# Kernel optimization log

Hardware: AMD Instinct MI355X
Metric: run time of the kernel (lower is better)

The kernel has to match this reference:

```python
import jax, jax.numpy as jnp
import numpy as np

B, S, D, H = 4, 2048, 1024, 16
HD = D // H
NEG = -1e30


def setup_inputs() -> dict:
    key = jax.random.key(0)
    ks = jax.random.split(key, 6)
    scale = 1.0 / np.sqrt(D)
    return {
        "q": jax.random.normal(ks[0], (B, S, D), jnp.float32),
        "k": jax.random.normal(ks[1], (B, S, D), jnp.float32),
        "v": jax.random.normal(ks[2], (B, S, D), jnp.float32),
        "mask": jnp.ones((B, 1, S), jnp.float32),
        "wq": jax.random.normal(ks[3], (D, D), jnp.float32) * scale,
        "bq": jnp.zeros((D,), jnp.float32),
        "wk": jax.random.normal(ks[4], (D, D), jnp.float32) * scale,
        "bk": jnp.zeros((D,), jnp.float32),
        "wv": jax.random.normal(ks[5], (D, D), jnp.float32) * scale,
        "bv": jnp.zeros((D,), jnp.float32),
    }


def _heads(x):
    # (B,S,D) -> (B,H,S,HD)
    return x.reshape(B, S, H, HD).transpose(0, 2, 1, 3)


def reference(q, k, v, mask, wq, bq, wk, bk, wv, bv):
    # pointwise Conv1D(kernel=1) == linear: x @ W^T + b (W: (out,in))
    qh = _heads(jnp.einsum('bsd,ed->bse', q, wq) + bq)
    kh = _heads(jnp.einsum('bsd,ed->bse', k, wk) + bk)
    vh = _heads(jnp.einsum('bsd,ed->bse', v, wv) + bv)
    scores = jnp.einsum('bhqd,bhkd->bhqk', qh, kh) / jnp.sqrt(jnp.float32(HD))
    # mask_logits: x + (1 - mask) * -1e30, mask (B,1,S) -> (B,1,1,S)
    scores = scores + (1.0 - mask[:, None, :, :]) * NEG
    probs = jax.nn.softmax(scores, axis=-1)  # dropout is identity in eval
    ctx = jnp.einsum('bhqk,bhkd->bhqd', probs, vh)
    return ctx.transpose(0, 2, 1, 3).reshape(B, S, D)
```

## Files before the change

kernel.cpp:

```cpp
#include <hip/hip_runtime.h>
#include <math.h>

typedef __attribute__((ext_vector_type(8)))  _Float16 f16x8;
typedef __attribute__((ext_vector_type(4)))  _Float16 f16x4;
typedef __attribute__((ext_vector_type(2)))  __fp16   h16x2;
typedef __attribute__((ext_vector_type(4)))  float    f32x4;
typedef __attribute__((ext_vector_type(16))) float    f32x16;
typedef unsigned int u32;

static constexpr int B  = 4;
static constexpr int S  = 2048;
static constexpr int D  = 1024;
static constexpr int H  = 16;
static constexpr int HD = 64;

#define CSCALE 0.18033688011112042f
#define MSHIFT -5.770780163555854f

union U64cvt { f16x4 h; ushort4 u; };
union W4 { u32 w[4]; f16x8 v; };

__device__ __forceinline__ void gld16(const void* g, void* l) {
    __builtin_amdgcn_global_load_lds((const u32*)g, (u32*)l, 16, 0, 0);
}

__device__ __forceinline__ void cvtwr16(const float4& x, const float4& y, void* dst) {
    W4 w;
    w.w[0] = __builtin_bit_cast(u32, __builtin_amdgcn_cvt_pkrtz(x.x, x.y));
    w.w[1] = __builtin_bit_cast(u32, __builtin_amdgcn_cvt_pkrtz(x.z, x.w));
    w.w[2] = __builtin_bit_cast(u32, __builtin_amdgcn_cvt_pkrtz(y.x, y.y));
    w.w[3] = __builtin_bit_cast(u32, __builtin_amdgcn_cvt_pkrtz(y.z, y.w));
    *(f16x8*)dst = w.v;
}

__global__ __launch_bounds__(256)
void cvt_prep(const float* __restrict__ q, const float* __restrict__ k,
              const float* __restrict__ v,
              const float* __restrict__ wq, const float* __restrict__ wk,
              const float* __restrict__ wv,
              unsigned short* __restrict__ dst)
{
    const int c = blockIdx.x * 256 + threadIdx.x;
    const float* src;
    size_t idx;
    if (c < 3145728) {
        const int a = c >> 20;
        src = (a == 0) ? q : (a == 1) ? k : v;
        idx = (size_t)(c & 1048575) * 8;
    } else {
        const int c2 = c - 3145728;
        const int a = c2 >> 17;
        src = (a == 0) ? wq : (a == 1) ? wk : wv;
        idx = (size_t)(c2 & 131071) * 8;
    }
    const float4 x = *(const float4*)(src + idx);
    const float4 y = *(const float4*)(src + idx + 4);
    cvtwr16(x, y, dst + (size_t)c * 8);
}

__global__ __launch_bounds__(256)
void mf_prep(const float* __restrict__ mask, unsigned short* __restrict__ mf)
{
    const int cm   = blockIdx.x * 256 + threadIdx.x;
    const int b    = cm >> 12;
    const int rem  = cm & 4095;
    const int t    = rem >> 7;
    const int kb   = (rem >> 6) & 1;
    const int lane = rem & 63;
    const int kv   = t * 64 + kb * 32 + (lane & 31);
    const float m  = fmaf(1.0f - mask[(size_t)b * S + kv], -30000.0f, MSHIFT);
    W4 w;
    w.w[0] = __builtin_bit_cast(u32, __builtin_amdgcn_cvt_pkrtz(m, 0.0f));
    w.w[1] = 0; w.w[2] = 0; w.w[3] = 0;
    *(f16x8*)(mf + (size_t)cm * 8) = w.v;
}

__global__ __launch_bounds__(256)
void proj_f16(const unsigned short* __restrict__ af16,
              const unsigned short* __restrict__ wf16,
              const float* __restrict__ bqp, const float* __restrict__ bkp,
              const float* __restrict__ bvp,
              unsigned short* __restrict__ outs)
{
    const int bid = blockIdx.x;
    const int xcd = bid & 7;
    const int idx = bid >> 3;
    const int z   = idx / 64;
    const int r2  = idx - z * 64;
    const int mpl = r2 >> 3;
    const int np  = r2 & 7;
    const int mp  = (xcd >> 1) * 16 + (xcd & 1) * 8 + mpl;
    const int m0  = mp * 128;
    const int n0  = np * 128;

    const unsigned short* A  = af16 + (size_t)z * 8388608;
    const unsigned short* Wf = wf16 + (size_t)z * 1048576;
    const float* bias = (z == 0) ? bqp : (z == 1) ? bkp : bvp;
    unsigned short* out = outs + (size_t)z * 8388608;

    const int tid  = threadIdx.x;
    const int lane = tid & 63;
    const int wid  = tid >> 6;
    const int wr   = wid >> 1;
    const int wc   = wid & 1;

    __shared__ __align__(16) unsigned char lA[2][8192];
    __shared__ __align__(16) unsigned char lB[2][8192];

    f32x4 acc[4][4];
#pragma unroll
    for (int i = 0; i < 4; ++i)
#pragma unroll
        for (int j = 0; j < 4; ++j) acc[i][j] = (f32x4){0.f, 0.f, 0.f, 0.f};

    int grow[2], gcol[2], lbase[2];
#pragma unroll
    for (int i = 0; i < 2; ++i) {
        const int c = tid + 256 * i;
        grow[i]  = c >> 2;
        gcol[i]  = ((c & 3) - (grow[i] >> 1)) & 3;
        lbase[i] = (c & ~63) * 16;
    }

#pragma unroll
    for (int i = 0; i < 2; ++i) {
        gld16(A  + (size_t)(m0 + grow[i]) * D + gcol[i] * 8, lA[0] + lbase[i]);
        gld16(Wf + (size_t)(n0 + grow[i]) * D + gcol[i] * 8, lB[0] + lbase[i]);
    }
    __syncthreads();

    for (int kt = 0; kt < 32; ++kt) {
        const int cb = kt & 1, nx = cb ^ 1;

        if (kt < 31) {
            const int k1 = (kt + 1) * 32;
#pragma unroll
            for (int i = 0; i < 2; ++i) {
                gld16(A  + (size_t)(m0 + grow[i]) * D + k1 + gcol[i] * 8, lA[nx] + lbase[i]);
                gld16(Wf + (size_t)(n0 + grow[i]) * D + k1 + gcol[i] * 8, lB[nx] + lbase[i]);
            }
        }

        f16x8 af[4], bf[4];
#pragma unroll
        for (int mi = 0; mi < 4; ++mi) {
            const int row = wr * 64 + mi * 16 + (lane & 15);
            const int cc  = ((lane >> 4) + (row >> 1)) & 3;
            af[mi] = *(const f16x8*)(lA[cb] + row * 64 + cc * 16);
        }
#pragma unroll
        for (int ni = 0; ni < 4; ++ni) {
            const int row = wc * 64 + ni * 16 + (lane & 15);
            const int cc  = ((lane >> 4) + (row >> 1)) & 3;
            bf[ni] = *(const f16x8*)(lB[cb] + row * 64 + cc * 16);
        }

        __builtin_amdgcn_s_setprio(1);
#pragma unroll
        for (int mi = 0; mi < 4; ++mi)
#pragma unroll
            for (int ni = 0; ni < 4; ++ni)
                acc[mi][ni] = __builtin_amdgcn_mfma_f32_16x16x32_f16(af[mi], bf[ni], acc[mi][ni], 0, 0, 0);
        __builtin_amdgcn_s_setprio(0);

        __syncthreads();
    }

#pragma unroll
    for (int mi = 0; mi < 4; ++mi) {
        const int gmBase = m0 + wr * 64 + mi * 16 + ((lane >> 4) << 2);
        const int b  = gmBase >> 11;
        const int s0 = gmBase & 2047;
        const int tV   = s0 >> 6;
        const int kv6  = s0 & 63;
        const int ksg  = kv6 >> 4;
        const int hi2v = (kv6 >> 3) & 1;
        const int jb   = kv6 & 7;
#pragma unroll
        for (int ni = 0; ni < 4; ++ni) {
            const int gn = n0 + wc * 64 + ni * 16 + (lane & 15);
            const float bb = bias[gn];
            const int hh = gn >> 6;
            const int hd = gn & 63;
            const size_t bhbase = ((size_t)b * H + hh) * ((size_t)S * HD);
            if (z == 0) {
#pragma unroll
                for (int r = 0; r < 4; ++r) {
                    const int gm = gmBase + r;
                    const _Float16 hv = (_Float16)((acc[mi][ni][r] + bb) * CSCALE);
                    out[bhbase + (size_t)(gm & 2047) * HD + hd] =
                        __builtin_bit_cast(unsigned short, hv);
                }
            } else if (z == 1) {
                const int ks   = hd >> 4;
                const int hi2k = (hd >> 3) & 1;
                const int j    = hd & 7;
#pragma unroll
                for (int r = 0; r < 4; ++r) {
                    const int s = (gmBase + r) & 2047;
                    const int t = s >> 6;
                    const int q = ((s >> 5) & 1) * 4 + ks;
                    const _Float16 hv = (_Float16)(acc[mi][ni][r] + bb);
                    out[bhbase + (((size_t)t * 8 + q) * 64 + hi2k * 32 + (s & 31)) * 8 + j] =
                        __builtin_bit_cast(unsigned short, hv);
                }
            } else {
                const int nb  = hd >> 5;
                const int c31 = hd & 31;
                const int q   = nb * 4 + ksg;
                U64cvt uu;
#pragma unroll
                for (int r = 0; r < 4; ++r)
                    uu.h[r] = (_Float16)(acc[mi][ni][r] + bb);
                *(ushort4*)(out + bhbase +
                    (((size_t)tV * 8 + q) * 64 + hi2v * 32 + c31) * 8 + jb) = uu.u;
            }
        }
    }
}

__global__ __launch_bounds__(256)
void proj_qkv(const float* __restrict__ qi, const float* __restrict__ ki,
              const float* __restrict__ vi,
              const float* __restrict__ wqp, const float* __restrict__ wkp,
              const float* __restrict__ wvp,
              const float* __restrict__ bqp, const float* __restrict__ bkp,
              const float* __restrict__ bvp,
              unsigned short* __restrict__ ws)
{
    const int bid = blockIdx.x;
    const int xcd = bid & 7;
    const int idx = bid >> 3;
    const int z   = idx / 64;
    const int r2  = idx - z * 64;
    const int mpl = r2 >> 3;
    const int np  = r2 & 7;
    const int mp  = (xcd >> 1) * 16 + (xcd & 1) * 8 + mpl;
    const int m0  = mp * 128;
    const int n0  = np * 128;

    const float* A    = (z == 0) ? qi  : (z == 1) ? ki  : vi;
    const float* W    = (z == 0) ? wqp : (z == 1) ? wkp : wvp;
    const float* bias = (z == 0) ? bqp : (z == 1) ? bkp : bvp;
    unsigned short* out = ws + (size_t)z * ((size_t)B * S * D);

    const int tid  = threadIdx.x;
    const int lane = tid & 63;
    const int wid  = tid >> 6;
    const int wr   = wid >> 1;
    const int wc   = wid & 1;

    __shared__ __align__(16) unsigned char lA[2][8192];
    __shared__ __align__(16) unsigned char lB[2][8192];

    f32x4 acc[4][4];
#pragma unroll
    for (int i = 0; i < 4; ++i)
#pragma unroll
        for (int j = 0; j < 4; ++j) acc[i][j] = (f32x4){0.f, 0.f, 0.f, 0.f};

    const int rb = (lane >> 4) * 16;

    int srow[2], sc8[2], soff[2];
#pragma unroll
    for (int i = 0; i < 2; ++i) {
        const int f = tid + 256 * i;
        srow[i] = f >> 2;
        sc8[i]  = f & 3;
        soff[i] = ((f >> 2) * 64 + (f & 3) * 16) ^ ((((f >> 2)) & 7) << 4);
    }

#pragma unroll
    for (int i = 0; i < 2; ++i) {
        const float* pa = A + (size_t)(m0 + srow[i]) * D + sc8[i] * 8;
        const float* pw = W + (size_t)(n0 + srow[i]) * D + sc8[i] * 8;
        cvtwr16(*(const float4*)pa, *(const float4*)(pa + 4), lA[0] + soff[i]);
        cvtwr16(*(const float4*)pw, *(const float4*)(pw + 4), lB[0] + soff[i]);
    }
    float4 pa0[2], pa1[2], pw0[2], pw1[2];
#pragma unroll
    for (int i = 0; i < 2; ++i) {
        const float* pa = A + (size_t)(m0 + srow[i]) * D + 32 + sc8[i] * 8;
        const float* pw = W + (size_t)(n0 + srow[i]) * D + 32 + sc8[i] * 8;
        pa0[i] = *(const float4*)pa;  pa1[i] = *(const float4*)(pa + 4);
        pw0[i] = *(const float4*)pw;  pw1[i] = *(const float4*)(pw + 4);
    }
    __syncthreads();

    for (int kt = 0; kt < 32; ++kt) {
        const int cb = kt & 1, nx = cb ^ 1;
        if (kt < 31) {
#pragma unroll
            for (int i = 0; i < 2; ++i) {
                cvtwr16(pa0[i], pa1[i], lA[nx] + soff[i]);
                cvtwr16(pw0[i], pw1[i], lB[nx] + soff[i]);
            }
        }
        f16x8 af[4], bf[4];
#pragma unroll
        for (int mi = 0; mi < 4; ++mi) {
            const int row = wr * 64 + mi * 16 + (lane & 15);
            af[mi] = *(const f16x8*)(lA[cb] + ((row * 64 + rb) ^ ((row & 7) << 4)));
        }
#pragma unroll
        for (int ni = 0; ni < 4; ++ni) {
            const int row = wc * 64 + ni * 16 + (lane & 15);
            bf[ni] = *(const f16x8*)(lB[cb] + ((row * 64 + rb) ^ ((row & 7) << 4)));
        }
        if (kt < 30) {
            const int k2 = (kt + 2) * 32;
#pragma unroll
            for (int i = 0; i < 2; ++i) {
                const float* pa = A + (size_t)(m0 + srow[i]) * D + k2 + sc8[i] * 8;
                const float* pw = W + (size_t)(n0 + srow[i]) * D + k2 + sc8[i] * 8;
                pa0[i] = *(const float4*)pa;  pa1[i] = *(const float4*)(pa + 4);
                pw0[i] = *(const float4*)pw;  pw1[i] = *(const float4*)(pw + 4);
            }
        }
        __builtin_amdgcn_s_setprio(1);
#pragma unroll
        for (int mi = 0; mi < 4; ++mi)
#pragma unroll
            for (int ni = 0; ni < 4; ++ni)
                acc[mi][ni] = __builtin_amdgcn_mfma_f32_16x16x32_f16(af[mi], bf[ni], acc[mi][ni], 0, 0, 0);
        __builtin_amdgcn_s_setprio(0);
        __syncthreads();
    }

#pragma unroll
    for (int mi = 0; mi < 4; ++mi) {
        const int gmBase = m0 + wr * 64 + mi * 16 + ((lane >> 4) << 2);
        const int b  = gmBase >> 11;
        const int s0 = gmBase & 2047;
        const int tV   = s0 >> 6;
        const int kv6  = s0 & 63;
        const int ksg  = kv6 >> 4;
        const int hi2v = (kv6 >> 3) & 1;
        const int jb   = kv6 & 7;
#pragma unroll
        for (int ni = 0; ni < 4; ++ni) {
            const int gn = n0 + wc * 64 + ni * 16 + (lane & 15);
            const float bb = bias[gn];
            const int hh = gn >> 6;
            const int hd = gn & 63;
            const size_t bhbase = ((size_t)b * H + hh) * ((size_t)S * HD);
            if (z == 0) {
#pragma unroll
                for (int r = 0; r < 4; ++r) {
                    const int gm = gmBase + r;
                    const _Float16 hv = (_Float16)((acc[mi][ni][r] + bb) * CSCALE);
                    out[bhbase + (size_t)(gm & 2047) * HD + hd] =
                        __builtin_bit_cast(unsigned short, hv);
                }
            } else if (z == 1) {
                const int ks   = hd >> 4;
                const int hi2k = (hd >> 3) & 1;
                const int j    = hd & 7;
#pragma unroll
                for (int r = 0; r < 4; ++r) {
                    const int s = (gmBase + r) & 2047;
                    const int t = s >> 6;
                    const int q = ((s >> 5) & 1) * 4 + ks;
                    const _Float16 hv = (_Float16)(acc[mi][ni][r] + bb);
                    out[bhbase + (((size_t)t * 8 + q) * 64 + hi2k * 32 + (s & 31)) * 8 + j] =
                        __builtin_bit_cast(unsigned short, hv);
                }
            } else {
                const int nb  = hd >> 5;
                const int c31 = hd & 31;
                const int q   = nb * 4 + ksg;
                U64cvt uu;
#pragma unroll
                for (int r = 0; r < 4; ++r)
                    uu.h[r] = (_Float16)(acc[mi][ni][r] + bb);
                *(ushort4*)(out + bhbase +
                    (((size_t)tV * 8 + q) * 64 + hi2v * 32 + c31) * 8 + jb) = uu.u;
            }
        }
    }
}

__global__ __launch_bounds__(256)
void attn_f16(const unsigned short* __restrict__ qh,
              const unsigned short* __restrict__ kf,
              const unsigned short* __restrict__ vf,
              const unsigned short* __restrict__ mf,
              float* __restrict__ out)
{
    const int flat = blockIdx.y * gridDim.x + blockIdx.x;
    const int sw   = (flat & 7) * 128 + (flat >> 3);
    const int bh   = sw >> 4;
    const int q0   = (sw & 15) * 128;

    const int b = bh >> 4;
    const int h = bh & 15;
    const unsigned short* Q  = qh + (size_t)bh * S * HD;
    const unsigned short* KF = kf + (size_t)bh * S * HD;
    const unsigned short* VF = vf + (size_t)bh * S * HD;
    const unsigned short* MFb = mf + (size_t)b * 32768;

    const int tid  = threadIdx.x;
    const int lane = tid & 63;
    const int wid  = tid >> 6;
    const int l31  = lane & 31;
    const int hi2  = lane >> 5;

    __shared__ __align__(16) unsigned char Kl[2][8192];
    __shared__ __align__(16) unsigned char Vl[2][8192];

    const int ldsA = wid * 1024;
    const int ldsB = wid * 1024 + 4096;
    const int g0   = tid * 8;
    const int g1   = tid * 8 + 2048;

    f16x8 aq[4];
    {
        const unsigned short* qrow = Q + (size_t)(q0 + wid * 32 + l31) * HD;
#pragma unroll
        for (int ks = 0; ks < 4; ++ks)
            aq[ks] = *(const f16x8*)(qrow + ks * 16 + hi2 * 8);
    }

    f16x8 aqone = {};
    if (hi2 == 0) aqone[0] = (_Float16)1.0f;

    f32x16 fzero = {};

    float ls0 = 0.f, ls1 = 0.f;
    f32x16 accO[2];
    accO[0] = (f32x16){};
    accO[1] = (f32x16){};
    const h16x2 one2 = {(__fp16)1.0f, (__fp16)1.0f};

    gld16(KF + g0, Kl[0] + ldsA);
    gld16(KF + g1, Kl[0] + ldsB);
    gld16(VF + g0, Vl[0] + ldsA);
    gld16(VF + g1, Vl[0] + ldsB);
    f16x8 mfc0 = *(const f16x8*)(MFb + lane * 8);
    f16x8 mfc1 = *(const f16x8*)(MFb + 512 + lane * 8);
    __syncthreads();

    const int lane16 = lane * 16;
    for (int t = 0; t < S / 64; ++t) {
        const int cb = t & 1, nx = cb ^ 1;
        const unsigned char* Kc = Kl[cb];
        const unsigned char* Vc = Vl[cb];

        f16x8 mfn0, mfn1;
        if (t < S / 64 - 1) {
            const int nt = (t + 1) * 4096;
            gld16(KF + nt + g0, Kl[nx] + ldsA);
            gld16(KF + nt + g1, Kl[nx] + ldsB);
            gld16(VF + nt + g0, Vl[nx] + ldsA);
            gld16(VF + nt + g1, Vl[nx] + ldsB);
            mfn0 = *(const f16x8*)(MFb + (t + 1) * 1024 + lane * 8);
            mfn1 = *(const f16x8*)(MFb + (t + 1) * 1024 + 512 + lane * 8);
        }

        f32x16 p[2];
        __builtin_amdgcn_s_setprio(1);
#pragma unroll
        for (int kb = 0; kb < 2; ++kb) {
            {
                const f16x8 ak = *(const f16x8*)(Kc + lane16 + (kb * 4 + 0) * 1024);
                p[kb] = __builtin_amdgcn_mfma_f32_32x32x16_f16(ak, aq[0], fzero, 0, 0, 0);
            }
#pragma unroll
            for (int ks = 1; ks < 4; ++ks) {
                const f16x8 ak = *(const f16x8*)(Kc + lane16 + (kb * 4 + ks) * 1024);
                p[kb] = __builtin_amdgcn_mfma_f32_32x32x16_f16(ak, aq[ks], p[kb], 0, 0, 0);
            }
            p[kb] = __builtin_amdgcn_mfma_f32_32x32x16_f16(kb == 0 ? mfc0 : mfc1, aqone, p[kb], 0, 0, 0);
        }
        __builtin_amdgcn_s_setprio(0);

        f16x8 pa[4];
#pragma unroll
        for (int kb = 0; kb < 2; ++kb) {
            float pe[16];
#pragma unroll
            for (int e = 0; e < 16; ++e)
                pe[e] = exp2f(p[kb][e]);
#pragma unroll
            for (int ks2 = 0; ks2 < 2; ++ks2) {
                const int o = ks2 * 8;
                const h16x2 h0 = __builtin_amdgcn_cvt_pkrtz(pe[o + 0], pe[o + 1]);
                const h16x2 h1 = __builtin_amdgcn_cvt_pkrtz(pe[o + 2], pe[o + 3]);
                const h16x2 h2 = __builtin_amdgcn_cvt_pkrtz(pe[o + 4], pe[o + 5]);
                const h16x2 h3 = __builtin_amdgcn_cvt_pkrtz(pe[o + 6], pe[o + 7]);
                ls0 = __builtin_amdgcn_fdot2(h0, one2, ls0, false);
                ls1 = __builtin_amdgcn_fdot2(h1, one2, ls1, false);
                ls0 = __builtin_amdgcn_fdot2(h2, one2, ls0, false);
                ls1 = __builtin_amdgcn_fdot2(h3, one2, ls1, false);
                u32 a0 = __builtin_bit_cast(u32, h0);
                u32 a1 = __builtin_bit_cast(u32, h1);
                u32 a2 = __builtin_bit_cast(u32, h2);
                u32 a3 = __builtin_bit_cast(u32, h3);
                asm volatile("v_permlane32_swap_b32 %0, %1" : "+v"(a0), "+v"(a2));
                asm volatile("v_permlane32_swap_b32 %0, %1" : "+v"(a1), "+v"(a3));
                W4 w;
                w.w[0] = a0; w.w[1] = a1; w.w[2] = a2; w.w[3] = a3;
                pa[kb * 2 + ks2] = w.v;
            }
        }

        __builtin_amdgcn_s_setprio(1);
#pragma unroll
        for (int nb = 0; nb < 2; ++nb)
#pragma unroll
            for (int ksg = 0; ksg < 4; ++ksg) {
                const f16x8 bv = *(const f16x8*)(Vc + lane16 + (nb * 4 + ksg) * 1024);
                accO[nb] = __builtin_amdgcn_mfma_f32_32x32x16_f16(pa[ksg], bv, accO[nb], 0, 0, 0);
            }
        __builtin_amdgcn_s_setprio(0);

        mfc0 = mfn0;
        mfc1 = mfn1;
        __syncthreads();
    }

    float lsum = ls0 + ls1;
    lsum += __shfl_xor(lsum, 32);
    const float linv = 1.0f / lsum;

    float lr[16];
#pragma unroll
    for (int r = 0; r < 16; ++r)
        lr[r] = __shfl(linv, (r & 3) + 8 * (r >> 2) + 4 * hi2);

#pragma unroll
    for (int nb = 0; nb < 2; ++nb) {
        const int dcol = h * HD + nb * 32 + l31;
#pragma unroll
        for (int r = 0; r < 16; ++r) {
            const int qrow = q0 + wid * 32 + (r & 3) + 8 * (r >> 2) + 4 * hi2;
            out[((size_t)b * S + qrow) * D + dcol] = accO[nb][r] * lr[r];
        }
    }
}

extern "C" void kernel_launch(void* const* d_in, const int* in_sizes, int n_in,
                              void* d_out, int out_size, void* d_ws, size_t ws_size,
                              hipStream_t stream)
{
    const float* q    = (const float*)d_in[0];
    const float* k    = (const float*)d_in[1];
    const float* v    = (const float*)d_in[2];
    const float* mask = (const float*)d_in[3];
    const float* wq   = (const float*)d_in[4];
    const float* bq   = (const float*)d_in[5];
    const float* wk   = (const float*)d_in[6];
    const float* bk   = (const float*)d_in[7];
    const float* wv   = (const float*)d_in[8];
    const float* bv   = (const float*)d_in[9];

    unsigned short* ws = (unsigned short*)d_ws;
    const size_t per  = (size_t)B * S * D;
    const size_t wsz  = 1048576;
    const size_t mfsz = 131072;
    const size_t need = (3 * per + 3 * wsz + 3 * per + mfsz) * 2;

    dim3 ga(S / 128, B * H);
    if (ws_size >= need) {
        unsigned short* af16 = ws;
        unsigned short* wf16 = ws + 3 * per;
        unsigned short* outs = ws + 3 * per + 3 * wsz;
        unsigned short* mfp  = outs + 3 * per;
        mf_prep<<<64, 256, 0, stream>>>(mask, mfp);
        cvt_prep<<<13824, 256, 0, stream>>>(q, k, v, wq, wk, wv, af16);
        proj_f16<<<1536, 256, 0, stream>>>(af16, wf16, bq, bk, bv, outs);
        attn_f16<<<ga, 256, 0, stream>>>(outs, outs + per, outs + 2 * per, mfp, (float*)d_out);
    } else {
        unsigned short* mfp = ws + 3 * per;
        mf_prep<<<64, 256, 0, stream>>>(mask, mfp);
        proj_qkv<<<1536, 256, 0, stream>>>(q, k, v, wq, wk, wv, bq, bk, bv, ws);
        attn_f16<<<ga, 256, 0, stream>>>(ws, ws + per, ws + 2 * per, mfp, (float*)d_out);
    }
}
```

Measured before the change: 230.0 us.

## Use 8-wave attention blocks and compute softmax row sums via MFMA

Doubles the attention block to 512 threads covering 256 query rows, so each K/V tile loaded into LDS is shared by twice as many waves and each thread issues half the global-to-LDS loads. Replaces the VALU fdot2 row-sum accumulation and the end-of-kernel shuffles with an extra MFMA of the probabilities against a ones vector, yielding sums already in the output layout. This adds matrix-core work per tile and halves the grid, which may hurt load balance across CUs.

```diff
diff --git a/kernel.cpp b/kernel.cpp
--- a/kernel.cpp
+++ b/kernel.cpp
@@ -380,7 +380,7 @@
     }
 }
 
-__global__ __launch_bounds__(256)
+__global__ __launch_bounds__(512)
 void attn_f16(const unsigned short* __restrict__ qh,
               const unsigned short* __restrict__ kf,
               const unsigned short* __restrict__ vf,
@@ -388,9 +388,9 @@
               float* __restrict__ out)
 {
     const int flat = blockIdx.y * gridDim.x + blockIdx.x;
-    const int sw   = (flat & 7) * 128 + (flat >> 3);
-    const int bh   = sw >> 4;
-    const int q0   = (sw & 15) * 128;
+    const int sw   = (flat & 7) * 64 + (flat >> 3);
+    const int bh   = sw >> 3;
+    const int q0   = (sw & 7) * 256;
 
     const int b = bh >> 4;
     const int h = bh & 15;
@@ -408,10 +408,8 @@
     __shared__ __align__(16) unsigned char Kl[2][8192];
     __shared__ __align__(16) unsigned char Vl[2][8192];
 
-    const int ldsA = wid * 1024;
-    const int ldsB = wid * 1024 + 4096;
+    const int ldsW = wid * 1024;
     const int g0   = tid * 8;
-    const int g1   = tid * 8 + 2048;
 
     f16x8 aq[4];
     {
@@ -423,19 +421,17 @@
 
     f16x8 aqone = {};
     if (hi2 == 0) aqone[0] = (_Float16)1.0f;
+    const f16x8 onesv = {(_Float16)1.f, (_Float16)1.f, (_Float16)1.f, (_Float16)1.f,
+                         (_Float16)1.f, (_Float16)1.f, (_Float16)1.f, (_Float16)1.f};
 
     f32x16 fzero = {};
-
-    float ls0 = 0.f, ls1 = 0.f;
-    f32x16 accO[2];
+    f32x16 accO[2], accL;
     accO[0] = (f32x16){};
     accO[1] = (f32x16){};
-    const h16x2 one2 = {(__fp16)1.0f, (__fp16)1.0f};
-
-    gld16(KF + g0, Kl[0] + ldsA);
-    gld16(KF + g1, Kl[0] + ldsB);
-    gld16(VF + g0, Vl[0] + ldsA);
-    gld16(VF + g1, Vl[0] + ldsB);
+    accL    = (f32x16){};
+
+    gld16(KF + g0, Kl[0] + ldsW);
+    gld16(VF + g0, Vl[0] + ldsW);
     f16x8 mfc0 = *(const f16x8*)(MFb + lane * 8);
     f16x8 mfc1 = *(const f16x8*)(MFb + 512 + lane * 8);
     __syncthreads();
@@ -449,10 +445,8 @@
         f16x8 mfn0, mfn1;
         if (t < S / 64 - 1) {
             const int nt = (t + 1) * 4096;
-            gld16(KF + nt + g0, Kl[nx] + ldsA);
-            gld16(KF + nt + g1, Kl[nx] + ldsB);
-            gld16(VF + nt + g0, Vl[nx] + ldsA);
-            gld16(VF + nt + g1, Vl[nx] + ldsB);
+            gld16(KF + nt + g0, Kl[nx] + ldsW);
+            gld16(VF + nt + g0, Vl[nx] + ldsW);
             mfn0 = *(const f16x8*)(MFb + (t + 1) * 1024 + lane * 8);
             mfn1 = *(const f16x8*)(MFb + (t + 1) * 1024 + 512 + lane * 8);
         }
@@ -484,18 +478,10 @@
 #pragma unroll
             for (int ks2 = 0; ks2 < 2; ++ks2) {
                 const int o = ks2 * 8;
-                const h16x2 h0 = __builtin_amdgcn_cvt_pkrtz(pe[o + 0], pe[o + 1]);
-                const h16x2 h1 = __builtin_amdgcn_cvt_pkrtz(pe[o + 2], pe[o + 3]);
-                const h16x2 h2 = __builtin_amdgcn_cvt_pkrtz(pe[o + 4], pe[o + 5]);
-                const h16x2 h3 = __builtin_amdgcn_cvt_pkrtz(pe[o + 6], pe[o + 7]);
-                ls0 = __builtin_amdgcn_fdot2(h0, one2, ls0, false);
-                ls1 = __builtin_amdgcn_fdot2(h1, one2, ls1, false);
-                ls0 = __builtin_amdgcn_fdot2(h2, one2, ls0, false);
-                ls1 = __builtin_amdgcn_fdot2(h3, one2, ls1, false);
-                u32 a0 = __builtin_bit_cast(u32, h0);
-                u32 a1 = __builtin_bit_cast(u32, h1);
-                u32 a2 = __builtin_bit_cast(u32, h2);
-                u32 a3 = __builtin_bit_cast(u32, h3);
+                u32 a0 = __builtin_bit_cast(u32, __builtin_amdgcn_cvt_pkrtz(pe[o + 0], pe[o + 1]));
+                u32 a1 = __builtin_bit_cast(u32, __builtin_amdgcn_cvt_pkrtz(pe[o + 2], pe[o + 3]));
+                u32 a2 = __builtin_bit_cast(u32, __builtin_amdgcn_cvt_pkrtz(pe[o + 4], pe[o + 5]));
+                u32 a3 = __builtin_bit_cast(u32, __builtin_amdgcn_cvt_pkrtz(pe[o + 6], pe[o + 7]));
                 asm volatile("v_permlane32_swap_b32 %0, %1" : "+v"(a0), "+v"(a2));
                 asm volatile("v_permlane32_swap_b32 %0, %1" : "+v"(a1), "+v"(a3));
                 W4 w;
@@ -512,6 +498,9 @@
                 const f16x8 bv = *(const f16x8*)(Vc + lane16 + (nb * 4 + ksg) * 1024);
                 accO[nb] = __builtin_amdgcn_mfma_f32_32x32x16_f16(pa[ksg], bv, accO[nb], 0, 0, 0);
             }
+#pragma unroll
+        for (int ksg = 0; ksg < 4; ++ksg)
+            accL = __builtin_amdgcn_mfma_f32_32x32x16_f16(pa[ksg], onesv, accL, 0, 0, 0);
         __builtin_amdgcn_s_setprio(0);
 
         mfc0 = mfn0;
@@ -519,22 +508,13 @@
         __syncthreads();
     }
 
-    float lsum = ls0 + ls1;
-    lsum += __shfl_xor(lsum, 32);
-    const float linv = 1.0f / lsum;
-
-    float lr[16];
-#pragma unroll
-    for (int r = 0; r < 16; ++r)
-        lr[r] = __shfl(linv, (r & 3) + 8 * (r >> 2) + 4 * hi2);
-
 #pragma unroll
     for (int nb = 0; nb < 2; ++nb) {
         const int dcol = h * HD + nb * 32 + l31;
 #pragma unroll
         for (int r = 0; r < 16; ++r) {
             const int qrow = q0 + wid * 32 + (r & 3) + 8 * (r >> 2) + 4 * hi2;
-            out[((size_t)b * S + qrow) * D + dcol] = accO[nb][r] * lr[r];
+            out[((size_t)b * S + qrow) * D + dcol] = accO[nb][r] / accL[r];
         }
     }
 }
@@ -560,7 +540,7 @@
     const size_t mfsz = 131072;
     const size_t need = (3 * per + 3 * wsz + 3 * per + mfsz) * 2;
 
-    dim3 ga(S / 128, B * H);
+    dim3 ga(S / 256, B * H);
     if (ws_size >= need) {
         unsigned short* af16 = ws;
         unsigned short* wf16 = ws + 3 * per;
@@ -569,11 +549,11 @@
         mf_prep<<<64, 256, 0, stream>>>(mask, mfp);
         cvt_prep<<<13824, 256, 0, stream>>>(q, k, v, wq, wk, wv, af16);
         proj_f16<<<1536, 256, 0, stream>>>(af16, wf16, bq, bk, bv, outs);
-        attn_f16<<<ga, 256, 0, stream>>>(outs, outs + per, outs + 2 * per, mfp, (float*)d_out);
+        attn_f16<<<ga, 512, 0, stream>>>(outs, outs + per, outs + 2 * per, mfp, (float*)d_out);
     } else {
         unsigned short* mfp = ws + 3 * per;
         mf_prep<<<64, 256, 0, stream>>>(mask, mfp);
         proj_qkv<<<1536, 256, 0, stream>>>(q, k, v, wq, wk, wv, bq, bk, bv, ws);
-        attn_f16<<<ga, 256, 0, stream>>>(ws, ws + per, ws + 2 * per, mfp, (float*)d_out);
-    }
-}
+        attn_f16<<<ga, 512, 0, stream>>>(ws, ws + per, ws + 2 * per, mfp, (float*)d_out);
+    }
+}
```

Result: no change. 227.7 us (-1.0%).
